# Optimization experiments

Measured on AMD Instinct MI355X. Metric: run time of the kernel, lower is better.

The kernel has to match this reference:

```python
import jax, jax.numpy as jnp
import numpy as np

B, L, D, H = 4, 2048, 1024, 16
DK = D // H  # 64


def setup_inputs() -> dict:
    key = jax.random.key(0)
    ks = jax.random.split(key, 5)
    x = jax.random.normal(ks[0], (B, L, D), dtype=jnp.float32)
    scale = 1.0 / np.sqrt(D)
    W_qkv = jax.random.normal(ks[1], (D, 3 * D), dtype=jnp.float32) * scale
    b_qkv = jnp.zeros((3 * D,), dtype=jnp.float32)
    W_out = jax.random.normal(ks[2], (D, D), dtype=jnp.float32) * scale
    b_out = jnp.zeros((D,), dtype=jnp.float32)
    return {"x": x, "W_qkv": W_qkv, "b_qkv": b_qkv, "W_out": W_out, "b_out": b_out}


def reference(x, W_qkv, b_qkv, W_out, b_out):
    Bx, Lx, Dx = x.shape
    qkv = x @ W_qkv + b_qkv                      # [B, L, 3D]
    q, k, v = jnp.split(qkv, 3, axis=-1)
    # [B, H, L, d_k]
    q = q.reshape(Bx, Lx, H, DK).transpose(0, 2, 1, 3)
    k = k.reshape(Bx, Lx, H, DK).transpose(0, 2, 1, 3)
    v = v.reshape(Bx, Lx, H, DK).transpose(0, 2, 1, 3)
    scores = jnp.einsum('bhqd,bhkd->bhqk', q, k) / np.sqrt(DK)
    causal = jnp.tril(jnp.ones((Lx, Lx), dtype=bool))
    scores = jnp.where(causal[None, None], scores, -jnp.inf)
    attn = jax.nn.softmax(scores, axis=-1)       # [B, H, L, L]
    out = jnp.einsum('bhqk,bhkd->bhqd', attn, v)
    out = out.transpose(0, 2, 1, 3).reshape(Bx, Lx, Dx)
    return out @ W_out + b_out
```

## Files before the change

kernel.cpp:

```cpp
#include <hip/hip_runtime.h>
#include <stdint.h>

#define B_ 4
#define L_ 2048
#define D_ 1024
#define H_ 16
#define DK_ 64

typedef __attribute__((ext_vector_type(8))) short bf16x8;
typedef __attribute__((ext_vector_type(4))) float f32x4;
typedef unsigned short bfu;

#define MFMA(a, b, c) __builtin_amdgcn_mfma_f32_16x16x32_bf16((a), (b), (c), 0, 0, 0)

__device__ __forceinline__ unsigned short f2bf(float f) {
  union { float f; unsigned int u; } v; v.f = f;
  unsigned int u = v.u;
  return (unsigned short)((u + 0x7fffu + ((u >> 16) & 1u)) >> 16);
}

__device__ __forceinline__ void gll16(const void* g, void* l) {
  __builtin_amdgcn_global_load_lds(
      (const __attribute__((address_space(1))) void*)g,
      (__attribute__((address_space(3))) void*)l, 16, 0, 0);
}

#define VMCNT(n_) asm volatile("s_waitcnt vmcnt(" #n_ ")" ::: "memory")
#define BARRIER() asm volatile("s_barrier" ::: "memory")


__global__ __launch_bounds__(256) void cast_x(const float* __restrict__ in,
                                              bfu* __restrict__ out, int n4) {
  int i = blockIdx.x * 256 + threadIdx.x;
  if (i >= n4) return;
  float4 v = ((const float4*)in)[i];
  ushort4 o;
  o.x = f2bf(v.x); o.y = f2bf(v.y); o.z = f2bf(v.z); o.w = f2bf(v.w);
  ((ushort4*)out)[i] = o;
}

__global__ __launch_bounds__(256) void wpack2(const float* __restrict__ in,
                                              bfu* __restrict__ out, int K, int C) {
  int idx = blockIdx.x * 256 + threadIdx.x;
  int c = idx % C, kb = idx / C;
  if (kb >= (K >> 3)) return;
  unsigned short v[8];
#pragma unroll
  for (int j = 0; j < 8; ++j) v[j] = f2bf(in[(size_t)(kb * 8 + j) * C + c]);
  size_t o = ((size_t)(c >> 4) * (K >> 3) + kb) * 128 + (c & 15) * 8;
  *(ushort4*)(out + o) = make_ushort4(v[0], v[1], v[2], v[3]);
  *(ushort4*)(out + o + 4) = make_ushort4(v[4], v[5], v[6], v[7]);
}


__global__ __launch_bounds__(256, 2) void gemm_n(
    const bfu* __restrict__ A, const bfu* __restrict__ Bp,
    const float* __restrict__ bias, bfu* __restrict__ Qg, bfu* __restrict__ Kg,
    bfu* __restrict__ Vtg, int M, int N, int K) {
  __shared__ __align__(16) bfu As[2][128 * 64];
  const int tid = threadIdx.x;
  const int lane = tid & 63;
  const int w = tid >> 6;
  const int wm = w >> 1, wn = w & 1;
  const int l15 = lane & 15, l4 = lane >> 4;

  const int nwg = gridDim.x;
  const int cpx = nwg >> 3;
  const int bid = (int)blockIdx.x;
  const int swz = (bid & 7) * cpx + (bid >> 3);
  const int NTt = N / 256;
  const int m0 = ((swz & 7) + 8 * (swz / (8 * NTt))) * 128;
  const int n0 = ((swz >> 3) % NTt) * 256;
  const int K8 = K >> 3;

  auto stageA = [&](int t) {
    char* lb = (char*)As[t & 1];
#pragma unroll
    for (int j = 0; j < 4; ++j) {
      int idx = j * 256 + tid;
      int row = idx >> 3, c16p = idx & 7, c16 = c16p ^ (row & 7);
      gll16(A + (size_t)(m0 + row) * K + t * 64 + c16 * 8,
            lb + row * 128 + c16p * 16);
    }
  };

  const size_t bbase = ((size_t)((n0 + wn * 128) >> 4)) * K8;
  auto loadB = [&](int t, int h, bf16x8 (&br)[4][2]) {
#pragma unroll
    for (int ni = 0; ni < 4; ++ni)
#pragma unroll
      for (int kk = 0; kk < 2; ++kk)
        br[ni][kk] = *(const bf16x8*)(
            Bp + (bbase + (size_t)(h * 4 + ni) * K8 + t * 8 + kk * 4 + l4) * 128 +
            l15 * 8);
  };

  f32x4 acc[4][8] = {};
  bf16x8 af[4][2], brX[4][2], brY[4][2];

  auto lda = [&](int t) {
    const char* base = (const char*)As[t & 1];
#pragma unroll
    for (int mi = 0; mi < 4; ++mi)
#pragma unroll
      for (int kk = 0; kk < 2; ++kk) {
        int row = wm * 64 + mi * 16 + l15;
        int ch = (kk * 4 + l4) ^ (row & 7);
        af[mi][kk] = *(const bf16x8*)(base + row * 128 + ch * 16);
      }
  };
  auto mm_half = [&](bf16x8 (&br)[4][2], int h) {
    __builtin_amdgcn_s_setprio(1);
#pragma unroll
    for (int kk = 0; kk < 2; ++kk)
#pragma unroll
      for (int mi = 0; mi < 4; ++mi)
#pragma unroll
        for (int ni = 0; ni < 4; ++ni)
          acc[mi][h * 4 + ni] = MFMA(af[mi][kk], br[ni][kk], acc[mi][h * 4 + ni]);
    __builtin_amdgcn_s_setprio(0);
  };

  const int NT = K >> 6;
  stageA(0);
  __builtin_amdgcn_sched_barrier(0);
  loadB(0, 0, brX);

  for (int t = 0; t < NT; ++t) {
    VMCNT(0); BARRIER();
    lda(t);
    loadB(t, 1, brY);
    if (t + 1 < NT) stageA(t + 1);
    __builtin_amdgcn_sched_barrier(0);
    mm_half(brX, 0);
    if (t + 1 < NT) loadB(t + 1, 0, brX);
    mm_half(brY, 1);
  }

  const int sec = n0 >> 10;
  if (sec < 2) {
    bfu* dst = (sec == 0) ? Qg : Kg;
    const float scale = (sec == 0) ? 0.18033688011112042f : 1.0f;
#pragma unroll
    for (int ni = 0; ni < 8; ++ni) {
      int gn = n0 + wn * 128 + ni * 16 + l15;
      int rem = gn & 1023;
      int hh = rem >> 6, dk = rem & 63;
      float bv = bias[gn];
#pragma unroll
      for (int mi = 0; mi < 4; ++mi)
#pragma unroll
        for (int rg = 0; rg < 4; ++rg) {
          int gm = m0 + wm * 64 + mi * 16 + l4 * 4 + rg;
          int bb = gm >> 11, ll = gm & 2047;
          dst[(((size_t)(bb * H_ + hh)) * L_ + ll) * DK_ + dk] =
              f2bf((acc[mi][ni][rg] + bv) * scale);
        }
    }
  } else {
    __syncthreads();
#pragma unroll
    for (int p = 0; p < 2; ++p) {
      if (wn == p) {
#pragma unroll
        for (int ni = 0; ni < 8; ++ni) {
          int n_rel = ni * 16 + l15;
          int gn = n0 + p * 128 + n_rel;
          float bv = bias[gn];
          int swzn = (n_rel & 7) << 4;
#pragma unroll
          for (int mi = 0; mi < 4; ++mi) {
            int m_base = wm * 64 + mi * 16 + l4 * 4;
            int k6 = m_base & 63;
            int p0 = (m_base & ~63) |
                     ((k6 & 32) | (((k6 >> 2) & 3) << 3) | (((k6 >> 4) & 1) << 2));
            float v0 = acc[mi][ni][0] + bv, v1 = acc[mi][ni][1] + bv;
            float v2 = acc[mi][ni][2] + bv, v3 = acc[mi][ni][3] + bv;
            uint32_t w01, w23;
            asm("v_cvt_pk_bf16_f32 %0, %1, %2" : "=v"(w01) : "v"(v0), "v"(v1));
            asm("v_cvt_pk_bf16_f32 %0, %1, %2" : "=v"(w23) : "v"(v2), "v"(v3));
            *(uint32_t*)((char*)As + n_rel * 256 + ((2 * p0) ^ swzn)) = w01;
            *(uint32_t*)((char*)As + n_rel * 256 + ((2 * p0 + 4) ^ swzn)) = w23;
          }
        }
      }
      __syncthreads();
      int n = tid >> 1;
      int cb = (tid & 1) * 8;
      int gnn = n0 + p * 128 + n;
      int hh = (gnn >> 6) & 15, dk = gnn & 63;
      size_t rowbase =
          (((size_t)((m0 >> 11) * H_ + hh)) * DK_ + dk) * L_ + (m0 & 2047);
#pragma unroll
      for (int j = 0; j < 8; ++j) {
        int ch = cb + j;
        bf16x8 vv = *(const bf16x8*)((char*)As + n * 256 +
                                     ((ch * 16) ^ ((n & 7) << 4)));
        *(bf16x8*)(Vtg + rowbase + ch * 8) = vv;
      }
      __syncthreads();
    }
  }
}


template <int EPI>
__global__ __launch_bounds__(256, 2) void gemm_r(
    const bfu* __restrict__ A, const bfu* __restrict__ Bp,
    const float* __restrict__ bias, bfu* __restrict__ Qg, bfu* __restrict__ Kg,
    bfu* __restrict__ Vtg, float* __restrict__ Out, int M, int N, int K) {
  __shared__ __align__(16) bfu As[2][128 * 64];
  const int tid = threadIdx.x;
  const int lane = tid & 63;
  const int w = tid >> 6;
  const int wm = w >> 1, wn = w & 1;
  const int l15 = lane & 15, l4 = lane >> 4;

  const int nwg = gridDim.x;
  const int cpx = nwg >> 3;
  const int bid = (int)blockIdx.x;
  const int swz = (bid & 7) * cpx + (bid >> 3);
  const int NTt = N / 128;
  const int m0 = ((swz & 7) + 8 * (swz / (8 * NTt))) * 128;
  const int n0 = ((swz >> 3) % NTt) * 128;
  const int K8 = K >> 3;

  auto stageA = [&](int t) {
    char* lb = (char*)As[t & 1];
#pragma unroll
    for (int j = 0; j < 4; ++j) {
      int idx = j * 256 + tid;
      int row = idx >> 3, c16p = idx & 7, c16 = c16p ^ (row & 7);
      gll16(A + (size_t)(m0 + row) * K + t * 64 + c16 * 8,
            lb + row * 128 + c16p * 16);
    }
  };

  const size_t bbase = ((size_t)((n0 + wn * 64) >> 4)) * K8;
  auto loadB = [&](int t, bf16x8 (&br)[4][2]) {
#pragma unroll
    for (int ni = 0; ni < 4; ++ni)
#pragma unroll
      for (int kk = 0; kk < 2; ++kk)
        br[ni][kk] = *(const bf16x8*)(
            Bp + (bbase + (size_t)ni * K8 + t * 8 + kk * 4 + l4) * 128 + l15 * 8);
  };

  f32x4 acc[4][4] = {};
  bf16x8 af[4][2], brA[4][2], brB[4][2];

  auto lda = [&](int t) {
    const char* base = (const char*)As[t & 1];
#pragma unroll
    for (int mi = 0; mi < 4; ++mi)
#pragma unroll
      for (int kk = 0; kk < 2; ++kk) {
        int row = wm * 64 + mi * 16 + l15;
        int ch = (kk * 4 + l4) ^ (row & 7);
        af[mi][kk] = *(const bf16x8*)(base + row * 128 + ch * 16);
      }
  };
  auto mm_all = [&](bf16x8 (&br)[4][2]) {
    __builtin_amdgcn_s_setprio(1);
#pragma unroll
    for (int kk = 0; kk < 2; ++kk)
#pragma unroll
      for (int mi = 0; mi < 4; ++mi)
#pragma unroll
        for (int ni = 0; ni < 4; ++ni)
          acc[mi][ni] = MFMA(af[mi][kk], br[ni][kk], acc[mi][ni]);
    __builtin_amdgcn_s_setprio(0);
  };

  const int NT = K >> 6;
  stageA(0);
  __builtin_amdgcn_sched_barrier(0);
  loadB(0, brA);
  loadB(1, brB);

  for (int t = 0; t < NT; t += 2) {
    VMCNT(8); BARRIER();
    lda(t);
    stageA(t + 1);
    __builtin_amdgcn_sched_barrier(0);
    mm_all(brA);
    if (t + 2 < NT) loadB(t + 2, brA);
    if (t + 2 < NT) { VMCNT(8); } else { VMCNT(0); }
    BARRIER();
    lda(t + 1);
    if (t + 2 < NT) stageA(t + 2);
    __builtin_amdgcn_sched_barrier(0);
    mm_all(brB);
    if (t + 3 < NT) loadB(t + 3, brB);
  }

  if constexpr (EPI == 1) {
#pragma unroll
    for (int ni = 0; ni < 4; ++ni) {
      int gn = n0 + wn * 64 + ni * 16 + l15;
      float bv = bias[gn];
#pragma unroll
      for (int mi = 0; mi < 4; ++mi)
#pragma unroll
        for (int rg = 0; rg < 4; ++rg) {
          int gm = m0 + wm * 64 + mi * 16 + l4 * 4 + rg;
          Out[(size_t)gm * N + gn] = acc[mi][ni][rg] + bv;
        }
    }
  }
}


__global__ __launch_bounds__(256, 3) void attn(const bfu* __restrict__ Qg,
                                               const bfu* __restrict__ Kg,
                                               const bfu* __restrict__ Vtg,
                                               bfu* __restrict__ Ao) {
  __shared__ __align__(16) bfu Ks[2 * 64 * 64];
  __shared__ __align__(16) bfu Vs[2 * 64 * 64];

  const int tid = threadIdx.x;
  const int lane = tid & 63;
  const int w = tid >> 6;
  const int l15 = lane & 15, l4 = lane >> 4;

  const int hid = blockIdx.x;
  const int xcd = hid & 7, slot = hid >> 3;
  const int bh = xcd * 8 + (slot >> 3);
  const int p = slot & 7;
  const int b = bh >> 4, h = bh & 15;

  for (int seg = 0; seg < 2; ++seg) {
    const int qb = (seg == 0) ? p : 15 - p;
    const int q0 = qb * 128;
    const int nt = 2 * qb + 2;
    const int q0w = q0 + w * 32;

    bf16x8 qf[2][2];
#pragma unroll
    for (int mi = 0; mi < 2; ++mi)
#pragma unroll
      for (int kk = 0; kk < 2; ++kk)
        qf[mi][kk] = *(const bf16x8*)(
            Qg + ((size_t)bh * L_ + q0w + mi * 16 + l15) * DK_ + kk * 32 + l4 * 8);

#pragma unroll
    for (int i = 0; i < 2; ++i) {
      int lb = i * 256 + tid;
      int r = lb >> 3, c16 = (lb & 7) ^ (r & 7);
      gll16(Kg + ((size_t)bh * L_ + r) * DK_ + c16 * 8, (char*)Ks + lb * 16);
      gll16(Vtg + ((size_t)bh * DK_ + r) * L_ + c16 * 8, (char*)Vs + lb * 16);
    }
    VMCNT(0);
    BARRIER();

    f32x4 acco[2][4] = {};
    float m[2] = {-1e30f, -1e30f};
    float l[2] = {0.f, 0.f};

    for (int t = 0; t < nt; ++t) {
      const int cur = t & 1;
      const int kv0 = t * 64;
      const char* Kc = (const char*)Ks + cur * 8192;
      const char* Vc = (const char*)Vs + cur * 8192;

      if (t + 1 < nt) {
        const int nb = (t + 1) & 1, nkv = (t + 1) * 64;
#pragma unroll
        for (int i = 0; i < 2; ++i) {
          int lb = i * 256 + tid;
          int r = lb >> 3, c16 = (lb & 7) ^ (r & 7);
          gll16(Kg + ((size_t)bh * L_ + nkv + r) * DK_ + c16 * 8,
                (char*)Ks + nb * 8192 + lb * 16);
          gll16(Vtg + ((size_t)bh * DK_ + r) * L_ + nkv + c16 * 8,
                (char*)Vs + nb * 8192 + lb * 16);
        }
        VMCNT(4);
      } else {
        VMCNT(0);
      }
      BARRIER();

      if (kv0 <= q0w + 31) {
        f32x4 s[2][4] = {};
        __builtin_amdgcn_s_setprio(1);
#pragma unroll
        for (int kk = 0; kk < 2; ++kk)
#pragma unroll
          for (int ni = 0; ni < 4; ++ni) {
            int r = ni * 16 + l15;
            int ch = (kk * 4 + l4) ^ (r & 7);
            bf16x8 kf = *(const bf16x8*)(Kc + r * 128 + ch * 16);
#pragma unroll
            for (int mi = 0; mi < 2; ++mi)
              s[mi][ni] = MFMA(kf, qf[mi][kk], s[mi][ni]);
          }
        __builtin_amdgcn_s_setprio(0);

        if (kv0 + 63 > q0w) {
#pragma unroll
          for (int mi = 0; mi < 2; ++mi) {
            int qg_ = q0w + mi * 16 + l15;
#pragma unroll
            for (int ni = 0; ni < 4; ++ni) {
              int kvg = kv0 + ni * 16 + l4 * 4;
#pragma unroll
              for (int rg = 0; rg < 4; ++rg)
                if (kvg + rg > qg_) s[mi][ni][rg] = -1e30f;
            }
          }
        }

        float mx[2];
#pragma unroll
        for (int mi = 0; mi < 2; ++mi) {
          float v = fmaxf(fmaxf(fmaxf(s[mi][0][0], s[mi][0][1]),
                                fmaxf(s[mi][0][2], s[mi][0][3])),
                          fmaxf(fmaxf(s[mi][1][0], s[mi][1][1]),
                                fmaxf(s[mi][1][2], s[mi][1][3])));
          v = fmaxf(v, fmaxf(fmaxf(fmaxf(s[mi][2][0], s[mi][2][1]),
                                   fmaxf(s[mi][2][2], s[mi][2][3])),
                             fmaxf(fmaxf(s[mi][3][0], s[mi][3][1]),
                                   fmaxf(s[mi][3][2], s[mi][3][3]))));
          v = fmaxf(v, __shfl_xor(v, 16));
          v = fmaxf(v, __shfl_xor(v, 32));
          mx[mi] = v;
        }
        float grow = fmaxf(mx[0] - m[0], mx[1] - m[1]);
        if (__any(grow > 11.0f)) {
#pragma unroll
          for (int mi = 0; mi < 2; ++mi) {
            float mn = fmaxf(m[mi], mx[mi]);
            float sc = __builtin_amdgcn_exp2f(m[mi] - mn);
            m[mi] = mn;
            l[mi] *= sc;
#pragma unroll
            for (int rg = 0; rg < 4; ++rg) {
              float scq = __shfl(sc, l4 * 4 + rg);
              acco[mi][0][rg] *= scq; acco[mi][1][rg] *= scq;
              acco[mi][2][rg] *= scq; acco[mi][3][rg] *= scq;
            }
          }
        }

        uint32_t pk[2][4][2];
#pragma unroll
        for (int mi = 0; mi < 2; ++mi)
#pragma unroll
          for (int ni = 0; ni < 4; ++ni) {
            float p0 = __builtin_amdgcn_exp2f(s[mi][ni][0] - m[mi]);
            float p1 = __builtin_amdgcn_exp2f(s[mi][ni][1] - m[mi]);
            float p2 = __builtin_amdgcn_exp2f(s[mi][ni][2] - m[mi]);
            float p3 = __builtin_amdgcn_exp2f(s[mi][ni][3] - m[mi]);
            l[mi] += (p0 + p1) + (p2 + p3);
            asm("v_cvt_pk_bf16_f32 %0, %1, %2" : "=v"(pk[mi][ni][0]) : "v"(p0), "v"(p1));
            asm("v_cvt_pk_bf16_f32 %0, %1, %2" : "=v"(pk[mi][ni][1]) : "v"(p2), "v"(p3));
          }

        __builtin_amdgcn_s_setprio(1);
#pragma unroll
        for (int kk = 0; kk < 2; ++kk) {
          union { uint32_t wd[4]; bf16x8 v; } u[2];
#pragma unroll
          for (int mi = 0; mi < 2; ++mi) {
            u[mi].wd[0] = pk[mi][2 * kk][0];
            u[mi].wd[1] = pk[mi][2 * kk][1];
            u[mi].wd[2] = pk[mi][2 * kk + 1][0];
            u[mi].wd[3] = pk[mi][2 * kk + 1][1];
          }
#pragma unroll
          for (int ni = 0; ni < 4; ++ni) {
            int r = ni * 16 + l15;
            int ch = (kk * 4 + l4) ^ (r & 7);
            bf16x8 vf = *(const bf16x8*)(Vc + r * 128 + ch * 16);
#pragma unroll
            for (int mi = 0; mi < 2; ++mi)
              acco[mi][ni] = MFMA(u[mi].v, vf, acco[mi][ni]);
          }
        }
        __builtin_amdgcn_s_setprio(0);
      }

      BARRIER();
    }

#pragma unroll
    for (int mi = 0; mi < 2; ++mi) {
      float ls = l[mi];
      ls += __shfl_xor(ls, 16);
      ls += __shfl_xor(ls, 32);
      float linv = 1.0f / ls;
#pragma unroll
      for (int rg = 0; rg < 4; ++rg) {
        float lq = __shfl(linv, l4 * 4 + rg);
        int q = q0w + mi * 16 + l4 * 4 + rg;
#pragma unroll
        for (int ni = 0; ni < 4; ++ni) {
          int d = ni * 16 + l15;
          Ao[((size_t)b * L_ + q) * D_ + h * DK_ + d] = f2bf(acco[mi][ni][rg] * lq);
        }
      }
    }
  }
}


extern "C" void kernel_launch(void* const* d_in, const int* in_sizes, int n_in,
                              void* d_out, int out_size, void* d_ws, size_t ws_size,
                              hipStream_t stream) {
  const float* x = (const float*)d_in[0];
  const float* W_qkv = (const float*)d_in[1];
  const float* b_qkv = (const float*)d_in[2];
  const float* W_out = (const float*)d_in[3];
  const float* b_out = (const float*)d_in[4];
  float* out = (float*)d_out;

  char* ws = (char*)d_ws;
  bfu* xb     = (bfu*)(ws);
  bfu* Wqkv_p = (bfu*)(ws + 16777216);
  bfu* Wout_p = (bfu*)(ws + 23068672);
  bfu* Qg     = (bfu*)(ws + 25165824);
  bfu* Kg     = (bfu*)(ws + 41943040);
  bfu* Vtg    = (bfu*)(ws + 58720256);
  bfu* Ao     = (bfu*)(ws + 75497472);

  cast_x<<<8192, 256, 0, stream>>>(x, xb, 2097152);
  wpack2<<<1536, 256, 0, stream>>>(W_qkv, Wqkv_p, 1024, 3072);
  wpack2<<<512, 256, 0, stream>>>(W_out, Wout_p, 1024, 1024);

  gemm_n<<<768, 256, 0, stream>>>(xb, Wqkv_p, b_qkv, Qg, Kg, Vtg, 8192, 3072, 1024);
  attn<<<512, 256, 0, stream>>>(Qg, Kg, Vtg, Ao);
  gemm_r<1><<<512, 256, 0, stream>>>(Ao, Wout_p, b_out, nullptr, nullptr, nullptr,
                                     out, 8192, 1024, 1024);
}
```

Baseline: 161.0 us.

## Retile QKV GEMM to 512-thread 256x128 blocks and split attention per q-block

The QKV projection GEMM now runs 512-thread workgroups on 256x128 output tiles with a fixed XCD-aware tile mapping. It reuses the double-buffered pipeline of the output GEMM and has a single-pass transposed V epilogue. The attention kernel no longer has each block process a balanced pair of query blocks serially. It launches 1024 blocks, one query block each, ordered longest causal workload first, with occupancy raised to 4 blocks per CU. This aims at better load balance and latency hiding, at the cost of less A-tile reuse per wave and more register pressure.

```diff
diff --git a/kernel.cpp b/kernel.cpp
--- a/kernel.cpp
+++ b/kernel.cpp
@@ -53,183 +53,28 @@
 }
 
 
-__global__ __launch_bounds__(256, 2) void gemm_n(
+__global__ __launch_bounds__(512, 2) void gemm_b(
     const bfu* __restrict__ A, const bfu* __restrict__ Bp,
     const float* __restrict__ bias, bfu* __restrict__ Qg, bfu* __restrict__ Kg,
     bfu* __restrict__ Vtg, int M, int N, int K) {
-  __shared__ __align__(16) bfu As[2][128 * 64];
+  __shared__ __align__(16) bfu As[2][256 * 64];
   const int tid = threadIdx.x;
   const int lane = tid & 63;
   const int w = tid >> 6;
   const int wm = w >> 1, wn = w & 1;
   const int l15 = lane & 15, l4 = lane >> 4;
 
-  const int nwg = gridDim.x;
-  const int cpx = nwg >> 3;
   const int bid = (int)blockIdx.x;
-  const int swz = (bid & 7) * cpx + (bid >> 3);
-  const int NTt = N / 256;
-  const int m0 = ((swz & 7) + 8 * (swz / (8 * NTt))) * 128;
-  const int n0 = ((swz >> 3) % NTt) * 256;
+  const int xcd = bid & 7, local = bid >> 3;
+  const int m0 = (xcd * 4 + (local & 3)) * 256;
+  const int n0 = (local >> 2) * 128;
   const int K8 = K >> 3;
 
   auto stageA = [&](int t) {
     char* lb = (char*)As[t & 1];
 #pragma unroll
     for (int j = 0; j < 4; ++j) {
-      int idx = j * 256 + tid;
-      int row = idx >> 3, c16p = idx & 7, c16 = c16p ^ (row & 7);
-      gll16(A + (size_t)(m0 + row) * K + t * 64 + c16 * 8,
-            lb + row * 128 + c16p * 16);
-    }
-  };
-
-  const size_t bbase = ((size_t)((n0 + wn * 128) >> 4)) * K8;
-  auto loadB = [&](int t, int h, bf16x8 (&br)[4][2]) {
-#pragma unroll
-    for (int ni = 0; ni < 4; ++ni)
-#pragma unroll
-      for (int kk = 0; kk < 2; ++kk)
-        br[ni][kk] = *(const bf16x8*)(
-            Bp + (bbase + (size_t)(h * 4 + ni) * K8 + t * 8 + kk * 4 + l4) * 128 +
-            l15 * 8);
-  };
-
-  f32x4 acc[4][8] = {};
-  bf16x8 af[4][2], brX[4][2], brY[4][2];
-
-  auto lda = [&](int t) {
-    const char* base = (const char*)As[t & 1];
-#pragma unroll
-    for (int mi = 0; mi < 4; ++mi)
-#pragma unroll
-      for (int kk = 0; kk < 2; ++kk) {
-        int row = wm * 64 + mi * 16 + l15;
-        int ch = (kk * 4 + l4) ^ (row & 7);
-        af[mi][kk] = *(const bf16x8*)(base + row * 128 + ch * 16);
-      }
-  };
-  auto mm_half = [&](bf16x8 (&br)[4][2], int h) {
-    __builtin_amdgcn_s_setprio(1);
-#pragma unroll
-    for (int kk = 0; kk < 2; ++kk)
-#pragma unroll
-      for (int mi = 0; mi < 4; ++mi)
-#pragma unroll
-        for (int ni = 0; ni < 4; ++ni)
-          acc[mi][h * 4 + ni] = MFMA(af[mi][kk], br[ni][kk], acc[mi][h * 4 + ni]);
-    __builtin_amdgcn_s_setprio(0);
-  };
-
-  const int NT = K >> 6;
-  stageA(0);
-  __builtin_amdgcn_sched_barrier(0);
-  loadB(0, 0, brX);
-
-  for (int t = 0; t < NT; ++t) {
-    VMCNT(0); BARRIER();
-    lda(t);
-    loadB(t, 1, brY);
-    if (t + 1 < NT) stageA(t + 1);
-    __builtin_amdgcn_sched_barrier(0);
-    mm_half(brX, 0);
-    if (t + 1 < NT) loadB(t + 1, 0, brX);
-    mm_half(brY, 1);
-  }
-
-  const int sec = n0 >> 10;
-  if (sec < 2) {
-    bfu* dst = (sec == 0) ? Qg : Kg;
-    const float scale = (sec == 0) ? 0.18033688011112042f : 1.0f;
-#pragma unroll
-    for (int ni = 0; ni < 8; ++ni) {
-      int gn = n0 + wn * 128 + ni * 16 + l15;
-      int rem = gn & 1023;
-      int hh = rem >> 6, dk = rem & 63;
-      float bv = bias[gn];
-#pragma unroll
-      for (int mi = 0; mi < 4; ++mi)
-#pragma unroll
-        for (int rg = 0; rg < 4; ++rg) {
-          int gm = m0 + wm * 64 + mi * 16 + l4 * 4 + rg;
-          int bb = gm >> 11, ll = gm & 2047;
-          dst[(((size_t)(bb * H_ + hh)) * L_ + ll) * DK_ + dk] =
-              f2bf((acc[mi][ni][rg] + bv) * scale);
-        }
-    }
-  } else {
-    __syncthreads();
-#pragma unroll
-    for (int p = 0; p < 2; ++p) {
-      if (wn == p) {
-#pragma unroll
-        for (int ni = 0; ni < 8; ++ni) {
-          int n_rel = ni * 16 + l15;
-          int gn = n0 + p * 128 + n_rel;
-          float bv = bias[gn];
-          int swzn = (n_rel & 7) << 4;
-#pragma unroll
-          for (int mi = 0; mi < 4; ++mi) {
-            int m_base = wm * 64 + mi * 16 + l4 * 4;
-            int k6 = m_base & 63;
-            int p0 = (m_base & ~63) |
-                     ((k6 & 32) | (((k6 >> 2) & 3) << 3) | (((k6 >> 4) & 1) << 2));
-            float v0 = acc[mi][ni][0] + bv, v1 = acc[mi][ni][1] + bv;
-            float v2 = acc[mi][ni][2] + bv, v3 = acc[mi][ni][3] + bv;
-            uint32_t w01, w23;
-            asm("v_cvt_pk_bf16_f32 %0, %1, %2" : "=v"(w01) : "v"(v0), "v"(v1));
-            asm("v_cvt_pk_bf16_f32 %0, %1, %2" : "=v"(w23) : "v"(v2), "v"(v3));
-            *(uint32_t*)((char*)As + n_rel * 256 + ((2 * p0) ^ swzn)) = w01;
-            *(uint32_t*)((char*)As + n_rel * 256 + ((2 * p0 + 4) ^ swzn)) = w23;
-          }
-        }
-      }
-      __syncthreads();
-      int n = tid >> 1;
-      int cb = (tid & 1) * 8;
-      int gnn = n0 + p * 128 + n;
-      int hh = (gnn >> 6) & 15, dk = gnn & 63;
-      size_t rowbase =
-          (((size_t)((m0 >> 11) * H_ + hh)) * DK_ + dk) * L_ + (m0 & 2047);
-#pragma unroll
-      for (int j = 0; j < 8; ++j) {
-        int ch = cb + j;
-        bf16x8 vv = *(const bf16x8*)((char*)As + n * 256 +
-                                     ((ch * 16) ^ ((n & 7) << 4)));
-        *(bf16x8*)(Vtg + rowbase + ch * 8) = vv;
-      }
-      __syncthreads();
-    }
-  }
-}
-
-
-template <int EPI>
-__global__ __launch_bounds__(256, 2) void gemm_r(
-    const bfu* __restrict__ A, const bfu* __restrict__ Bp,
-    const float* __restrict__ bias, bfu* __restrict__ Qg, bfu* __restrict__ Kg,
-    bfu* __restrict__ Vtg, float* __restrict__ Out, int M, int N, int K) {
-  __shared__ __align__(16) bfu As[2][128 * 64];
-  const int tid = threadIdx.x;
-  const int lane = tid & 63;
-  const int w = tid >> 6;
-  const int wm = w >> 1, wn = w & 1;
-  const int l15 = lane & 15, l4 = lane >> 4;
-
-  const int nwg = gridDim.x;
-  const int cpx = nwg >> 3;
-  const int bid = (int)blockIdx.x;
-  const int swz = (bid & 7) * cpx + (bid >> 3);
-  const int NTt = N / 128;
-  const int m0 = ((swz & 7) + 8 * (swz / (8 * NTt))) * 128;
-  const int n0 = ((swz >> 3) % NTt) * 128;
-  const int K8 = K >> 3;
-
-  auto stageA = [&](int t) {
-    char* lb = (char*)As[t & 1];
-#pragma unroll
-    for (int j = 0; j < 4; ++j) {
-      int idx = j * 256 + tid;
+      int idx = j * 512 + tid;
       int row = idx >> 3, c16p = idx & 7, c16 = c16p ^ (row & 7);
       gll16(A + (size_t)(m0 + row) * K + t * 64 + c16 * 8,
             lb + row * 128 + c16p * 16);
@@ -294,24 +139,171 @@
     if (t + 3 < NT) loadB(t + 3, brB);
   }
 
-  if constexpr (EPI == 1) {
+  const int sec = n0 >> 10;
+  if (sec < 2) {
+    bfu* dst = (sec == 0) ? Qg : Kg;
+    const float scale = (sec == 0) ? 0.18033688011112042f : 1.0f;
 #pragma unroll
     for (int ni = 0; ni < 4; ++ni) {
       int gn = n0 + wn * 64 + ni * 16 + l15;
+      int rem = gn & 1023;
+      int hh = rem >> 6, dk = rem & 63;
       float bv = bias[gn];
 #pragma unroll
       for (int mi = 0; mi < 4; ++mi)
 #pragma unroll
         for (int rg = 0; rg < 4; ++rg) {
           int gm = m0 + wm * 64 + mi * 16 + l4 * 4 + rg;
-          Out[(size_t)gm * N + gn] = acc[mi][ni][rg] + bv;
-        }
-    }
-  }
-}
-
-
-__global__ __launch_bounds__(256, 3) void attn(const bfu* __restrict__ Qg,
+          int bb = gm >> 11, ll = gm & 2047;
+          dst[(((size_t)(bb * H_ + hh)) * L_ + ll) * DK_ + dk] =
+              f2bf((acc[mi][ni][rg] + bv) * scale);
+        }
+    }
+  } else {
+    __syncthreads();
+#pragma unroll
+    for (int ni = 0; ni < 4; ++ni) {
+      int n_local = wn * 64 + ni * 16 + l15;
+      int gn = n0 + n_local;
+      float bv = bias[gn];
+      int swzn = (n_local & 7) << 4;
+#pragma unroll
+      for (int mi = 0; mi < 4; ++mi) {
+        int m_base = wm * 64 + mi * 16 + l4 * 4;
+        int k6 = m_base & 63;
+        int p0 = (m_base & ~63) |
+                 ((k6 & 32) | (((k6 >> 2) & 3) << 3) | (((k6 >> 4) & 1) << 2));
+        float v0 = acc[mi][ni][0] + bv, v1 = acc[mi][ni][1] + bv;
+        float v2 = acc[mi][ni][2] + bv, v3 = acc[mi][ni][3] + bv;
+        uint32_t w01, w23;
+        asm("v_cvt_pk_bf16_f32 %0, %1, %2" : "=v"(w01) : "v"(v0), "v"(v1));
+        asm("v_cvt_pk_bf16_f32 %0, %1, %2" : "=v"(w23) : "v"(v2), "v"(v3));
+        *(uint32_t*)((char*)As + n_local * 512 + ((2 * p0) ^ swzn)) = w01;
+        *(uint32_t*)((char*)As + n_local * 512 + ((2 * p0 + 4) ^ swzn)) = w23;
+      }
+    }
+    __syncthreads();
+    int n = tid >> 2;
+    int cb = (tid & 3) * 8;
+    int gnn = n0 + n;
+    int hh = (gnn >> 6) & 15, dk = gnn & 63;
+    size_t rowbase =
+        (((size_t)((m0 >> 11) * H_ + hh)) * DK_ + dk) * L_ + (m0 & 2047);
+#pragma unroll
+    for (int j = 0; j < 8; ++j) {
+      int ch = cb + j;
+      bf16x8 vv = *(const bf16x8*)((char*)As + n * 512 +
+                                   ((ch * 16) ^ ((n & 7) << 4)));
+      *(bf16x8*)(Vtg + rowbase + ch * 8) = vv;
+    }
+  }
+}
+
+
+__global__ __launch_bounds__(256, 2) void gemm_r(
+    const bfu* __restrict__ A, const bfu* __restrict__ Bp,
+    const float* __restrict__ bias, float* __restrict__ Out, int M, int N, int K) {
+  __shared__ __align__(16) bfu As[2][128 * 64];
+  const int tid = threadIdx.x;
+  const int lane = tid & 63;
+  const int w = tid >> 6;
+  const int wm = w >> 1, wn = w & 1;
+  const int l15 = lane & 15, l4 = lane >> 4;
+
+  const int nwg = gridDim.x;
+  const int cpx = nwg >> 3;
+  const int bid = (int)blockIdx.x;
+  const int swz = (bid & 7) * cpx + (bid >> 3);
+  const int NTt = N / 128;
+  const int m0 = ((swz & 7) + 8 * (swz / (8 * NTt))) * 128;
+  const int n0 = ((swz >> 3) % NTt) * 128;
+  const int K8 = K >> 3;
+
+  auto stageA = [&](int t) {
+    char* lb = (char*)As[t & 1];
+#pragma unroll
+    for (int j = 0; j < 4; ++j) {
+      int idx = j * 256 + tid;
+      int row = idx >> 3, c16p = idx & 7, c16 = c16p ^ (row & 7);
+      gll16(A + (size_t)(m0 + row) * K + t * 64 + c16 * 8,
+            lb + row * 128 + c16p * 16);
+    }
+  };
+
+  const size_t bbase = ((size_t)((n0 + wn * 64) >> 4)) * K8;
+  auto loadB = [&](int t, bf16x8 (&br)[4][2]) {
+#pragma unroll
+    for (int ni = 0; ni < 4; ++ni)
+#pragma unroll
+      for (int kk = 0; kk < 2; ++kk)
+        br[ni][kk] = *(const bf16x8*)(
+            Bp + (bbase + (size_t)ni * K8 + t * 8 + kk * 4 + l4) * 128 + l15 * 8);
+  };
+
+  f32x4 acc[4][4] = {};
+  bf16x8 af[4][2], brA[4][2], brB[4][2];
+
+  auto lda = [&](int t) {
+    const char* base = (const char*)As[t & 1];
+#pragma unroll
+    for (int mi = 0; mi < 4; ++mi)
+#pragma unroll
+      for (int kk = 0; kk < 2; ++kk) {
+        int row = wm * 64 + mi * 16 + l15;
+        int ch = (kk * 4 + l4) ^ (row & 7);
+        af[mi][kk] = *(const bf16x8*)(base + row * 128 + ch * 16);
+      }
+  };
+  auto mm_all = [&](bf16x8 (&br)[4][2]) {
+    __builtin_amdgcn_s_setprio(1);
+#pragma unroll
+    for (int kk = 0; kk < 2; ++kk)
+#pragma unroll
+      for (int mi = 0; mi < 4; ++mi)
+#pragma unroll
+        for (int ni = 0; ni < 4; ++ni)
+          acc[mi][ni] = MFMA(af[mi][kk], br[ni][kk], acc[mi][ni]);
+    __builtin_amdgcn_s_setprio(0);
+  };
+
+  const int NT = K >> 6;
+  stageA(0);
+  __builtin_amdgcn_sched_barrier(0);
+  loadB(0, brA);
+  loadB(1, brB);
+
+  for (int t = 0; t < NT; t += 2) {
+    VMCNT(8); BARRIER();
+    lda(t);
+    stageA(t + 1);
+    __builtin_amdgcn_sched_barrier(0);
+    mm_all(brA);
+    if (t + 2 < NT) loadB(t + 2, brA);
+    if (t + 2 < NT) { VMCNT(8); } else { VMCNT(0); }
+    BARRIER();
+    lda(t + 1);
+    if (t + 2 < NT) stageA(t + 2);
+    __builtin_amdgcn_sched_barrier(0);
+    mm_all(brB);
+    if (t + 3 < NT) loadB(t + 3, brB);
+  }
+
+#pragma unroll
+  for (int ni = 0; ni < 4; ++ni) {
+    int gn = n0 + wn * 64 + ni * 16 + l15;
+    float bv = bias[gn];
+#pragma unroll
+    for (int mi = 0; mi < 4; ++mi)
+#pragma unroll
+      for (int rg = 0; rg < 4; ++rg) {
+        int gm = m0 + wm * 64 + mi * 16 + l4 * 4 + rg;
+        Out[(size_t)gm * N + gn] = acc[mi][ni][rg] + bv;
+      }
+  }
+}
+
+
+__global__ __launch_bounds__(256, 4) void attn(const bfu* __restrict__ Qg,
                                                const bfu* __restrict__ Kg,
                                                const bfu* __restrict__ Vtg,
                                                bfu* __restrict__ Ao) {
@@ -323,181 +315,178 @@
   const int w = tid >> 6;
   const int l15 = lane & 15, l4 = lane >> 4;
 
-  const int hid = blockIdx.x;
-  const int xcd = hid & 7, slot = hid >> 3;
-  const int bh = xcd * 8 + (slot >> 3);
-  const int p = slot & 7;
+  const int bid = (int)blockIdx.x;
+  const int g = bid >> 8, r = bid & 255;
+  const int qb = 15 - 4 * g - ((r + g) & 3);
+  const int bh = r >> 2;
   const int b = bh >> 4, h = bh & 15;
 
-  for (int seg = 0; seg < 2; ++seg) {
-    const int qb = (seg == 0) ? p : 15 - p;
-    const int q0 = qb * 128;
-    const int nt = 2 * qb + 2;
-    const int q0w = q0 + w * 32;
-
-    bf16x8 qf[2][2];
-#pragma unroll
-    for (int mi = 0; mi < 2; ++mi)
+  const int q0 = qb * 128;
+  const int nt = 2 * qb + 2;
+  const int q0w = q0 + w * 32;
+
+  bf16x8 qf[2][2];
+#pragma unroll
+  for (int mi = 0; mi < 2; ++mi)
+#pragma unroll
+    for (int kk = 0; kk < 2; ++kk)
+      qf[mi][kk] = *(const bf16x8*)(
+          Qg + ((size_t)bh * L_ + q0w + mi * 16 + l15) * DK_ + kk * 32 + l4 * 8);
+
+#pragma unroll
+  for (int i = 0; i < 2; ++i) {
+    int lb = i * 256 + tid;
+    int rr = lb >> 3, c16 = (lb & 7) ^ (rr & 7);
+    gll16(Kg + ((size_t)bh * L_ + rr) * DK_ + c16 * 8, (char*)Ks + lb * 16);
+    gll16(Vtg + ((size_t)bh * DK_ + rr) * L_ + c16 * 8, (char*)Vs + lb * 16);
+  }
+  VMCNT(0);
+  BARRIER();
+
+  f32x4 acco[2][4] = {};
+  float m[2] = {-1e30f, -1e30f};
+  float l[2] = {0.f, 0.f};
+
+  for (int t = 0; t < nt; ++t) {
+    const int cur = t & 1;
+    const int kv0 = t * 64;
+    const char* Kc = (const char*)Ks + cur * 8192;
+    const char* Vc = (const char*)Vs + cur * 8192;
+
+    if (t + 1 < nt) {
+      const int nb = (t + 1) & 1, nkv = (t + 1) * 64;
+#pragma unroll
+      for (int i = 0; i < 2; ++i) {
+        int lb = i * 256 + tid;
+        int rr = lb >> 3, c16 = (lb & 7) ^ (rr & 7);
+        gll16(Kg + ((size_t)bh * L_ + nkv + rr) * DK_ + c16 * 8,
+              (char*)Ks + nb * 8192 + lb * 16);
+        gll16(Vtg + ((size_t)bh * DK_ + rr) * L_ + nkv + c16 * 8,
+              (char*)Vs + nb * 8192 + lb * 16);
+      }
+      VMCNT(4);
+    } else {
+      VMCNT(0);
+    }
+    BARRIER();
+
+    if (kv0 <= q0w + 31) {
+      f32x4 s[2][4] = {};
+      __builtin_amdgcn_s_setprio(1);
 #pragma unroll
       for (int kk = 0; kk < 2; ++kk)
-        qf[mi][kk] = *(const bf16x8*)(
-            Qg + ((size_t)bh * L_ + q0w + mi * 16 + l15) * DK_ + kk * 32 + l4 * 8);
-
-#pragma unroll
-    for (int i = 0; i < 2; ++i) {
-      int lb = i * 256 + tid;
-      int r = lb >> 3, c16 = (lb & 7) ^ (r & 7);
-      gll16(Kg + ((size_t)bh * L_ + r) * DK_ + c16 * 8, (char*)Ks + lb * 16);
-      gll16(Vtg + ((size_t)bh * DK_ + r) * L_ + c16 * 8, (char*)Vs + lb * 16);
-    }
-    VMCNT(0);
+#pragma unroll
+        for (int ni = 0; ni < 4; ++ni) {
+          int rr = ni * 16 + l15;
+          int ch = (kk * 4 + l4) ^ (rr & 7);
+          bf16x8 kf = *(const bf16x8*)(Kc + rr * 128 + ch * 16);
+#pragma unroll
+          for (int mi = 0; mi < 2; ++mi)
+            s[mi][ni] = MFMA(kf, qf[mi][kk], s[mi][ni]);
+        }
+      __builtin_amdgcn_s_setprio(0);
+
+      if (kv0 + 63 > q0w) {
+#pragma unroll
+        for (int mi = 0; mi < 2; ++mi) {
+          int qg_ = q0w + mi * 16 + l15;
+#pragma unroll
+          for (int ni = 0; ni < 4; ++ni) {
+            int kvg = kv0 + ni * 16 + l4 * 4;
+#pragma unroll
+            for (int rg = 0; rg < 4; ++rg)
+              if (kvg + rg > qg_) s[mi][ni][rg] = -1e30f;
+          }
+        }
+      }
+
+      float mx[2];
+#pragma unroll
+      for (int mi = 0; mi < 2; ++mi) {
+        float v = fmaxf(fmaxf(fmaxf(s[mi][0][0], s[mi][0][1]),
+                              fmaxf(s[mi][0][2], s[mi][0][3])),
+                        fmaxf(fmaxf(s[mi][1][0], s[mi][1][1]),
+                              fmaxf(s[mi][1][2], s[mi][1][3])));
+        v = fmaxf(v, fmaxf(fmaxf(fmaxf(s[mi][2][0], s[mi][2][1]),
+                                 fmaxf(s[mi][2][2], s[mi][2][3])),
+                           fmaxf(fmaxf(s[mi][3][0], s[mi][3][1]),
+                                 fmaxf(s[mi][3][2], s[mi][3][3]))));
+        v = fmaxf(v, __shfl_xor(v, 16));
+        v = fmaxf(v, __shfl_xor(v, 32));
+        mx[mi] = v;
+      }
+      float grow = fmaxf(mx[0] - m[0], mx[1] - m[1]);
+      if (__any(grow > 11.0f)) {
+#pragma unroll
+        for (int mi = 0; mi < 2; ++mi) {
+          float mn = fmaxf(m[mi], mx[mi]);
+          float sc = __builtin_amdgcn_exp2f(m[mi] - mn);
+          m[mi] = mn;
+          l[mi] *= sc;
+#pragma unroll
+          for (int rg = 0; rg < 4; ++rg) {
+            float scq = __shfl(sc, l4 * 4 + rg);
+            acco[mi][0][rg] *= scq; acco[mi][1][rg] *= scq;
+            acco[mi][2][rg] *= scq; acco[mi][3][rg] *= scq;
+          }
+        }
+      }
+
+      uint32_t pk[2][4][2];
+#pragma unroll
+      for (int mi = 0; mi < 2; ++mi)
+#pragma unroll
+        for (int ni = 0; ni < 4; ++ni) {
+          float p0 = __builtin_amdgcn_exp2f(s[mi][ni][0] - m[mi]);
+          float p1 = __builtin_amdgcn_exp2f(s[mi][ni][1] - m[mi]);
+          float p2 = __builtin_amdgcn_exp2f(s[mi][ni][2] - m[mi]);
+          float p3 = __builtin_amdgcn_exp2f(s[mi][ni][3] - m[mi]);
+          l[mi] += (p0 + p1) + (p2 + p3);
+          asm("v_cvt_pk_bf16_f32 %0, %1, %2" : "=v"(pk[mi][ni][0]) : "v"(p0), "v"(p1));
+          asm("v_cvt_pk_bf16_f32 %0, %1, %2" : "=v"(pk[mi][ni][1]) : "v"(p2), "v"(p3));
+        }
+
+      __builtin_amdgcn_s_setprio(1);
+#pragma unroll
+      for (int kk = 0; kk < 2; ++kk) {
+        union { uint32_t wd[4]; bf16x8 v; } u[2];
+#pragma unroll
+        for (int mi = 0; mi < 2; ++mi) {
+          u[mi].wd[0] = pk[mi][2 * kk][0];
+          u[mi].wd[1] = pk[mi][2 * kk][1];
+          u[mi].wd[2] = pk[mi][2 * kk + 1][0];
+          u[mi].wd[3] = pk[mi][2 * kk + 1][1];
+        }
+#pragma unroll
+        for (int ni = 0; ni < 4; ++ni) {
+          int rr = ni * 16 + l15;
+          int ch = (kk * 4 + l4) ^ (rr & 7);
+          bf16x8 vf = *(const bf16x8*)(Vc + rr * 128 + ch * 16);
+#pragma unroll
+          for (int mi = 0; mi < 2; ++mi)
+            acco[mi][ni] = MFMA(u[mi].v, vf, acco[mi][ni]);
+        }
+      }
+      __builtin_amdgcn_s_setprio(0);
+    }
+
     BARRIER();
-
-    f32x4 acco[2][4] = {};
-    float m[2] = {-1e30f, -1e30f};
-    float l[2] = {0.f, 0.f};
-
-    for (int t = 0; t < nt; ++t) {
-      const int cur = t & 1;
-      const int kv0 = t * 64;
-      const char* Kc = (const char*)Ks + cur * 8192;
-      const char* Vc = (const char*)Vs + cur * 8192;
-
-      if (t + 1 < nt) {
-        const int nb = (t + 1) & 1, nkv = (t + 1) * 64;
-#pragma unroll
-        for (int i = 0; i < 2; ++i) {
-          int lb = i * 256 + tid;
-          int r = lb >> 3, c16 = (lb & 7) ^ (r & 7);
-          gll16(Kg + ((size_t)bh * L_ + nkv + r) * DK_ + c16 * 8,
-                (char*)Ks + nb * 8192 + lb * 16);
-          gll16(Vtg + ((size_t)bh * DK_ + r) * L_ + nkv + c16 * 8,
-                (char*)Vs + nb * 8192 + lb * 16);
-        }
-        VMCNT(4);
-      } else {
-        VMCNT(0);
-      }
-      BARRIER();
-
-      if (kv0 <= q0w + 31) {
-        f32x4 s[2][4] = {};
-        __builtin_amdgcn_s_setprio(1);
-#pragma unroll
-        for (int kk = 0; kk < 2; ++kk)
-#pragma unroll
-          for (int ni = 0; ni < 4; ++ni) {
-            int r = ni * 16 + l15;
-            int ch = (kk * 4 + l4) ^ (r & 7);
-            bf16x8 kf = *(const bf16x8*)(Kc + r * 128 + ch * 16);
-#pragma unroll
-            for (int mi = 0; mi < 2; ++mi)
-              s[mi][ni] = MFMA(kf, qf[mi][kk], s[mi][ni]);
-          }
-        __builtin_amdgcn_s_setprio(0);
-
-        if (kv0 + 63 > q0w) {
-#pragma unroll
-          for (int mi = 0; mi < 2; ++mi) {
-            int qg_ = q0w + mi * 16 + l15;
-#pragma unroll
-            for (int ni = 0; ni < 4; ++ni) {
-              int kvg = kv0 + ni * 16 + l4 * 4;
-#pragma unroll
-              for (int rg = 0; rg < 4; ++rg)
-                if (kvg + rg > qg_) s[mi][ni][rg] = -1e30f;
-            }
-          }
-        }
-
-        float mx[2];
-#pragma unroll
-        for (int mi = 0; mi < 2; ++mi) {
-          float v = fmaxf(fmaxf(fmaxf(s[mi][0][0], s[mi][0][1]),
-                                fmaxf(s[mi][0][2], s[mi][0][3])),
-                          fmaxf(fmaxf(s[mi][1][0], s[mi][1][1]),
-                                fmaxf(s[mi][1][2], s[mi][1][3])));
-          v = fmaxf(v, fmaxf(fmaxf(fmaxf(s[mi][2][0], s[mi][2][1]),
-                                   fmaxf(s[mi][2][2], s[mi][2][3])),
-                             fmaxf(fmaxf(s[mi][3][0], s[mi][3][1]),
-                                   fmaxf(s[mi][3][2], s[mi][3][3]))));
-          v = fmaxf(v, __shfl_xor(v, 16));
-          v = fmaxf(v, __shfl_xor(v, 32));
-          mx[mi] = v;
-        }
-        float grow = fmaxf(mx[0] - m[0], mx[1] - m[1]);
-        if (__any(grow > 11.0f)) {
-#pragma unroll
-          for (int mi = 0; mi < 2; ++mi) {
-            float mn = fmaxf(m[mi], mx[mi]);
-            float sc = __builtin_amdgcn_exp2f(m[mi] - mn);
-            m[mi] = mn;
-            l[mi] *= sc;
-#pragma unroll
-            for (int rg = 0; rg < 4; ++rg) {
-              float scq = __shfl(sc, l4 * 4 + rg);
-              acco[mi][0][rg] *= scq; acco[mi][1][rg] *= scq;
-              acco[mi][2][rg] *= scq; acco[mi][3][rg] *= scq;
-            }
-          }
-        }
-
-        uint32_t pk[2][4][2];
-#pragma unroll
-        for (int mi = 0; mi < 2; ++mi)
-#pragma unroll
-          for (int ni = 0; ni < 4; ++ni) {
-            float p0 = __builtin_amdgcn_exp2f(s[mi][ni][0] - m[mi]);
-            float p1 = __builtin_amdgcn_exp2f(s[mi][ni][1] - m[mi]);
-            float p2 = __builtin_amdgcn_exp2f(s[mi][ni][2] - m[mi]);
-            float p3 = __builtin_amdgcn_exp2f(s[mi][ni][3] - m[mi]);
-            l[mi] += (p0 + p1) + (p2 + p3);
-            asm("v_cvt_pk_bf16_f32 %0, %1, %2" : "=v"(pk[mi][ni][0]) : "v"(p0), "v"(p1));
-            asm("v_cvt_pk_bf16_f32 %0, %1, %2" : "=v"(pk[mi][ni][1]) : "v"(p2), "v"(p3));
-          }
-
-        __builtin_amdgcn_s_setprio(1);
-#pragma unroll
-        for (int kk = 0; kk < 2; ++kk) {
-          union { uint32_t wd[4]; bf16x8 v; } u[2];
-#pragma unroll
-          for (int mi = 0; mi < 2; ++mi) {
-            u[mi].wd[0] = pk[mi][2 * kk][0];
-            u[mi].wd[1] = pk[mi][2 * kk][1];
-            u[mi].wd[2] = pk[mi][2 * kk + 1][0];
-            u[mi].wd[3] = pk[mi][2 * kk + 1][1];
-          }
-#pragma unroll
-          for (int ni = 0; ni < 4; ++ni) {
-            int r = ni * 16 + l15;
-            int ch = (kk * 4 + l4) ^ (r & 7);
-            bf16x8 vf = *(const bf16x8*)(Vc + r * 128 + ch * 16);
-#pragma unroll
-            for (int mi = 0; mi < 2; ++mi)
-              acco[mi][ni] = MFMA(u[mi].v, vf, acco[mi][ni]);
-          }
-        }
-        __builtin_amdgcn_s_setprio(0);
-      }
-
-      BARRIER();
-    }
-
-#pragma unroll
-    for (int mi = 0; mi < 2; ++mi) {
-      float ls = l[mi];
-      ls += __shfl_xor(ls, 16);
-      ls += __shfl_xor(ls, 32);
-      float linv = 1.0f / ls;
-#pragma unroll
-      for (int rg = 0; rg < 4; ++rg) {
-        float lq = __shfl(linv, l4 * 4 + rg);
-        int q = q0w + mi * 16 + l4 * 4 + rg;
-#pragma unroll
-        for (int ni = 0; ni < 4; ++ni) {
-          int d = ni * 16 + l15;
-          Ao[((size_t)b * L_ + q) * D_ + h * DK_ + d] = f2bf(acco[mi][ni][rg] * lq);
-        }
+  }
+
+#pragma unroll
+  for (int mi = 0; mi < 2; ++mi) {
+    float ls = l[mi];
+    ls += __shfl_xor(ls, 16);
+    ls += __shfl_xor(ls, 32);
+    float linv = 1.0f / ls;
+#pragma unroll
+    for (int rg = 0; rg < 4; ++rg) {
+      float lq = __shfl(linv, l4 * 4 + rg);
+      int q = q0w + mi * 16 + l4 * 4 + rg;
+#pragma unroll
+      for (int ni = 0; ni < 4; ++ni) {
+        int d = ni * 16 + l15;
+        Ao[((size_t)b * L_ + q) * D_ + h * DK_ + d] = f2bf(acco[mi][ni][rg] * lq);
       }
     }
   }
@@ -527,8 +516,7 @@
   wpack2<<<1536, 256, 0, stream>>>(W_qkv, Wqkv_p, 1024, 3072);
   wpack2<<<512, 256, 0, stream>>>(W_out, Wout_p, 1024, 1024);
 
-  gemm_n<<<768, 256, 0, stream>>>(xb, Wqkv_p, b_qkv, Qg, Kg, Vtg, 8192, 3072, 1024);
-  attn<<<512, 256, 0, stream>>>(Qg, Kg, Vtg, Ao);
-  gemm_r<1><<<512, 256, 0, stream>>>(Ao, Wout_p, b_out, nullptr, nullptr, nullptr,
-                                     out, 8192, 1024, 1024);
-}
+  gemm_b<<<768, 512, 0, stream>>>(xb, Wqkv_p, b_qkv, Qg, Kg, Vtg, 8192, 3072, 1024);
+  attn<<<1024, 256, 0, stream>>>(Qg, Kg, Vtg, Ao);
+  gemm_r<<<512, 256, 0, stream>>>(Ao, Wout_p, b_out, out, 8192, 1024, 1024);
+}
```

Measured after the change: 173.7 us. 1.08x slower.
